# Kernel tuning notes

Measured on AMD Instinct MI355X. Metric: run time of the kernel, lower is better.

Reference implementation:

```python
import jax, jax.numpy as jnp
import numpy as np

N, K, P, D, H = 1024, 32, 1024, 512, 256
FDIM = 3 * P + 3 * D + 4  # 4612
GLOBAL_MEAN_AFFINITY = 6.5


def _init_linear(key, fan_in, fan_out):
    kw, kb = jax.random.split(key)
    bound = 1.0 / np.sqrt(fan_in)
    w = jax.random.uniform(kw, (fan_in, fan_out), jnp.float32, -bound, bound)
    b = jax.random.uniform(kb, (fan_out,), jnp.float32, -bound, bound)
    return w, b


def setup_inputs() -> dict:
    key = jax.random.key(0)
    ks = jax.random.split(key, 16)
    inp = {
        "neighbor_protein": jax.random.normal(ks[0], (N, K, P), jnp.float32),
        "neighbor_drug": jax.random.normal(ks[1], (N, K, D), jnp.float32),
        "neighbor_affinity": jax.random.normal(ks[2], (N, K), jnp.float32),
        "neighbor_ppr": jax.random.uniform(ks[3], (N, K), jnp.float32),
        "neighbor_trust": jax.random.uniform(ks[4], (N, K), jnp.float32),
        "neighbor_mask": jax.random.randint(ks[5], (N, K), 0, 2).astype(bool),
        "qry_protein": jax.random.normal(ks[6], (N, P), jnp.float32),
        "qry_drug": jax.random.normal(ks[7], (N, D), jnp.float32),
    }
    # weight_net params
    inp["w1"], inp["wb1"] = _init_linear(ks[8], FDIM, H)
    inp["w2"], inp["wb2"] = _init_linear(ks[9], H, H // 2)
    inp["w3"], inp["wb3"] = _init_linear(ks[10], H // 2, 1)
    # delta_net params
    inp["d1"], inp["db1"] = _init_linear(ks[11], FDIM, H)
    inp["d2"], inp["db2"] = _init_linear(ks[12], H, H // 2)
    inp["d3"], inp["db3"] = _init_linear(ks[13], H // 2, 1)
    # binding_encoder params (MLP over [qry_protein, qry_drug])
    inp["be1"], inp["beb1"] = _init_linear(ks[14], P + D, H)
    inp["be2"], inp["beb2"] = _init_linear(ks[15], H, 1)
    inp["log_sigma"] = jnp.zeros((1,), jnp.float32)
    return inp


def _mlp3(x, w1, b1, w2, b2, w3, b3):
    h = jax.nn.relu(x @ w1 + b1)
    h = jax.nn.relu(h @ w2 + b2)
    return (h @ w3 + b3)[..., 0]


def _cosine_sim(a, b, eps=1e-8):
    na = jnp.maximum(jnp.linalg.norm(a, axis=-1), eps)
    nb = jnp.maximum(jnp.linalg.norm(b, axis=-1), eps)
    return jnp.sum(a * b, axis=-1) / (na * nb)


def reference(neighbor_protein, neighbor_drug, neighbor_affinity, neighbor_ppr,
              neighbor_trust, neighbor_mask, qry_protein, qry_drug,
              w1, wb1, w2, wb2, w3, wb3,
              d1, db1, d2, db2, d3, db3,
              be1, beb1, be2, beb2, log_sigma):
    # --- feature build: [N, K, FDIM] ---
    qp = jnp.broadcast_to(qry_protein[:, None, :], neighbor_protein.shape)
    qd = jnp.broadcast_to(qry_drug[:, None, :], neighbor_drug.shape)
    drug_sim = _cosine_sim(qd, neighbor_drug)  # [N, K]
    features = jnp.concatenate([
        qp, neighbor_protein, qp - neighbor_protein,
        qd, neighbor_drug, qd - neighbor_drug,
        neighbor_affinity[..., None], neighbor_ppr[..., None],
        neighbor_trust[..., None], drug_sim[..., None],
    ], axis=-1)

    # --- weight net + masked softmax over K ---
    logits = _mlp3(features, w1, wb1, w2, wb2, w3, wb3)  # [N, K]
    logits = jnp.where(neighbor_mask, logits, -1e9)
    weights = jax.nn.softmax(logits, axis=1) * neighbor_mask.astype(jnp.float32)
    norm = jnp.sum(weights, axis=1, keepdims=True)
    weights = jnp.where(norm > 0, weights / jnp.maximum(norm, 1e-8),
                        jnp.zeros_like(weights))

    transfer = jnp.sum(weights * neighbor_affinity, axis=1)  # [N]
    delta = _mlp3(features, d1, db1, d2, db2, d3, db3)  # [N, K]
    correction = jnp.sum(weights * delta, axis=1)  # [N]

    # --- binding encoder prior ---
    be_in = jnp.concatenate([qry_protein, qry_drug], axis=-1)
    prior = (jax.nn.relu(be_in @ be1 + beb1) @ be2 + beb2)[..., 0] + GLOBAL_MEAN_AFFINITY

    has_neighbors = jnp.any(neighbor_mask, axis=1)  # [N]
    mu = jnp.where(has_neighbors, transfer + correction, prior)
    base_sigma = jnp.broadcast_to(jax.nn.softplus(log_sigma), mu.shape)
    sigma = base_sigma + (~has_neighbors).astype(jnp.float32) * 0.15 + 1e-4
    return mu, sigma
```

## Files before the change

### kernel.cpp

```cpp
#include <hip/hip_runtime.h>
#include <cstdint>
#include <cstddef>


typedef __attribute__((ext_vector_type(8))) short s16x8;
typedef __attribute__((ext_vector_type(4))) float f32x4;

static __device__ __forceinline__ unsigned short f2bf(float f) {
  unsigned u = __float_as_uint(f);
  u += 0x7fffu + ((u >> 16) & 1u);
  return (unsigned short)(u >> 16);
}

static __device__ __forceinline__ void glds16(const void* g, void* l) {
  __builtin_amdgcn_global_load_lds(
      (const __attribute__((address_space(1))) void*)g,
      (__attribute__((address_space(3))) void*)l, 16, 0, 0);
}

__global__ void prep_k(const float* __restrict__ qp, const float* __restrict__ qd,
                       unsigned short* __restrict__ Aq, float* __restrict__ qn,
                       const float* __restrict__ w1, const float* __restrict__ d1,
                       const float* __restrict__ be1, const float* __restrict__ w2,
                       const float* __restrict__ d2,
                       unsigned short* __restrict__ Bt1,
                       unsigned short* __restrict__ Btq,
                       unsigned short* __restrict__ Bt2c) {
  const int t = threadIdx.x;
  if (blockIdx.x < 1024) {
    const int n = blockIdx.x;
    const float4* qp4 = (const float4*)(qp + (size_t)n * 1024);
    float4 v = qp4[t];
    ushort4 o4;
    o4.x = f2bf(v.x); o4.y = f2bf(v.y); o4.z = f2bf(v.z); o4.w = f2bf(v.w);
    *(ushort4*)(Aq + (size_t)n * 1536 + t * 4) = o4;
    const float2* qd2 = (const float2*)(qd + (size_t)n * 512);
    float2 w = qd2[t];
    ushort2 o2; o2.x = f2bf(w.x); o2.y = f2bf(w.y);
    *(ushort2*)(Aq + (size_t)n * 1536 + 1024 + t * 2) = o2;
    float ss = w.x * w.x + w.y * w.y;
    #pragma unroll
    for (int m = 32; m >= 1; m >>= 1) ss += __shfl_xor(ss, m);
    __shared__ float sr[4];
    if ((t & 63) == 0) sr[t >> 6] = ss;
    __syncthreads();
    if (t == 0) qn[n] = sqrtf(sr[0] + sr[1] + sr[2] + sr[3]);
    return;
  }
  const int NB1 = 512 * 1536, NBQ = 768 * 1536, NB2 = 256 * 256;
  const int nb = gridDim.x - 1024;
  for (int idx = (blockIdx.x - 1024) * 256 + t; idx < NB1 + NBQ + NB2;
       idx += nb * 256) {
    if (idx < NB1) {
      int c = idx / 1536, j = idx - c * 1536;
      const float* W = (c < 256) ? w1 : d1;
      int cc = c & 255;
      float v;
      if (j < 1024) v = W[(1024 + j) * 256 + cc] - W[(2048 + j) * 256 + cc];
      else { int jd = j - 1024; v = W[(3584 + jd) * 256 + cc] - W[(4096 + jd) * 256 + cc]; }
      Bt1[idx] = f2bf(v);
    } else if (idx < NB1 + NBQ) {
      int i2 = idx - NB1;
      int c = i2 / 1536, j = i2 - c * 1536;
      float v;
      if (c < 512) {
        const float* W = (c < 256) ? w1 : d1;
        int cc = c & 255;
        if (j < 1024) v = W[j * 256 + cc] + W[(2048 + j) * 256 + cc];
        else { int jd = j - 1024; v = W[(3072 + jd) * 256 + cc] + W[(4096 + jd) * 256 + cc]; }
      } else {
        v = be1[j * 256 + (c - 512)];
      }
      Btq[i2] = f2bf(v);
    } else {
      int i2 = idx - NB1 - NBQ;
      int o = i2 >> 8, j = i2 & 255;
      float v = (o < 128) ? w2[j * 128 + o] : d2[j * 128 + (o - 128)];
      Bt2c[i2] = f2bf(v);
    }
  }
}

__global__ __launch_bounds__(256) void gemm0_k(
    const unsigned short* __restrict__ abf, const unsigned short* __restrict__ Bt,
    const float* __restrict__ wb1, const float* __restrict__ db1,
    const float* __restrict__ beb1, float* __restrict__ uq_out) {
  __shared__ short As[128 * 64];
  __shared__ short Bs[128 * 64];
  const int tid = threadIdx.x;
  const int l = tid & 63, w = tid >> 6;
  const int wr = w >> 1, wc = w & 1;
  const int br = blockIdx.x, bc = blockIdx.y;
  const int c0 = bc * 128;
  f32x4 acc[4][4] = {};

  for (int kt = 0; kt < 24; ++kt) {
    const int k0 = kt * 64;
    __syncthreads();
    #pragma unroll
    for (int rep = 0; rep < 4; ++rep) {
      int q = rep * 256 + tid;
      int row = q >> 3, slot = q & 7;
      int kc = slot ^ (row & 7);
      int gk = k0 + kc * 8;
      long grow = (long)br * 128 + row;
      s16x8 pk = *(const s16x8*)(abf + grow * 1536 + gk);
      *(s16x8*)(&As[q * 8]) = pk;
      s16x8 pb = *(const s16x8*)(Bt + (long)(c0 + row) * 1536 + gk);
      *(s16x8*)(&Bs[q * 8]) = pb;
    }
    __syncthreads();
    #pragma unroll
    for (int kh = 0; kh < 2; ++kh) {
      s16x8 af[4], bfr[4];
      #pragma unroll
      for (int mi = 0; mi < 4; ++mi) {
        int ra = wr * 64 + mi * 16 + (l & 15);
        int sidx = (kh * 4 + (l >> 4)) ^ (ra & 7);
        af[mi] = *(const s16x8*)(&As[ra * 64 + sidx * 8]);
      }
      #pragma unroll
      for (int ni = 0; ni < 4; ++ni) {
        int rb = wc * 64 + ni * 16 + (l & 15);
        int sidx = (kh * 4 + (l >> 4)) ^ (rb & 7);
        bfr[ni] = *(const s16x8*)(&Bs[rb * 64 + sidx * 8]);
      }
      #pragma unroll
      for (int mi = 0; mi < 4; ++mi)
        #pragma unroll
        for (int ni = 0; ni < 4; ++ni)
          acc[mi][ni] = __builtin_amdgcn_mfma_f32_16x16x32_bf16(
              af[mi], bfr[ni], acc[mi][ni], 0, 0, 0);
    }
  }
  #pragma unroll
  for (int mi = 0; mi < 4; ++mi)
    #pragma unroll
    for (int ni = 0; ni < 4; ++ni)
      #pragma unroll
      for (int r = 0; r < 4; ++r) {
        int rowl = wr * 64 + mi * 16 + (l >> 4) * 4 + r;
        int coll = wc * 64 + ni * 16 + (l & 15);
        long grow = (long)br * 128 + rowl;
        int gcol = c0 + coll;
        float b = (gcol < 256) ? wb1[gcol]
                 : (gcol < 512) ? db1[gcol - 256] : beb1[gcol - 512];
        uq_out[grow * 768 + gcol] = acc[mi][ni][r] + b;
      }
}

__global__ __launch_bounds__(512, 2) void gemm1_k(
    const float* __restrict__ Anp, const float* __restrict__ And,
    const unsigned short* __restrict__ Bt,
    const float* __restrict__ uq, const float* __restrict__ aff,
    const float* __restrict__ ppr, const float* __restrict__ trs,
    const float* __restrict__ qd, const float* __restrict__ qn,
    const float* __restrict__ w1, const float* __restrict__ d1,
    const unsigned short* __restrict__ Bt2c,
    const float* __restrict__ wb2, const float* __restrict__ db2,
    const float* __restrict__ w3, const float* __restrict__ wb3,
    const float* __restrict__ d3, const float* __restrict__ db3,
    float* __restrict__ ld) {
  __shared__ short As[2][128 * 64];
  __shared__ short Bs[2][512 * 64];
  const int tid = threadIdx.x;
  const int l = tid & 63, w = tid >> 6;
  const int wr = w >> 2, wc = w & 3;
  const long br = blockIdx.x;
  const int arow = tid >> 2, aseg = tid & 3;
  const long agrow = br * 128 + arow;
  const long an = agrow >> 5;
  const int brow = tid >> 3, bslot = tid & 7;
  const int lc = l & 15, lk = l >> 4;

  f32x4 acc[4][8] = {};
  float areg[16], qreg[16];
  float dotp = 0.f, nsp = 0.f;

  auto stageBhalf = [&](int buf, int kt, int h) {
    const int k0 = kt * 64;
    #pragma unroll
    for (int i = 0; i < 4; ++i) {
      int idx = h * 4 + i;
      int row = idx * 64 + brow;
      const unsigned short* src =
          Bt + (size_t)row * 1536 + k0 + ((bslot ^ (row & 7)) * 8);
      glds16(src, &Bs[buf][(idx * 512 + tid) * 8]);
    }
  };
  auto loadA = [&](int kt) {
    const int k0 = kt * 64 + aseg * 16;
    const float* src = (k0 < 1024) ? (Anp + agrow * 1024 + k0)
                                   : (And + agrow * 512 + (k0 - 1024));
    #pragma unroll
    for (int i = 0; i < 4; ++i) {
      float4 v = ((const float4*)src)[i];
      areg[i * 4 + 0] = v.x; areg[i * 4 + 1] = v.y;
      areg[i * 4 + 2] = v.z; areg[i * 4 + 3] = v.w;
    }
    if (kt >= 16) {
      const float* qs = qd + an * 512 + (k0 - 1024);
      #pragma unroll
      for (int i = 0; i < 4; ++i) {
        float4 v = ((const float4*)qs)[i];
        qreg[i * 4 + 0] = v.x; qreg[i * 4 + 1] = v.y;
        qreg[i * 4 + 2] = v.z; qreg[i * 4 + 3] = v.w;
      }
    }
  };
  auto writeA = [&](int buf, int kt) {
    if (kt >= 16) {
      #pragma unroll
      for (int j = 0; j < 16; ++j) {
        dotp += areg[j] * qreg[j];
        nsp  += areg[j] * areg[j];
      }
    }
    #pragma unroll
    for (int j = 0; j < 2; ++j) {
      int slot = (aseg * 2 + j) ^ (arow & 7);
      s16x8 pk;
      #pragma unroll
      for (int e = 0; e < 8; ++e) pk[e] = (short)f2bf(areg[j * 8 + e]);
      *(s16x8*)(&As[buf][arow * 64 + slot * 8]) = pk;
    }
  };

  auto rdA = [&](int cur, int kh, s16x8* af) {
    #pragma unroll
    for (int mi = 0; mi < 4; ++mi) {
      int ra = wr * 64 + mi * 16 + lc;
      int sl = (kh * 4 + lk) ^ (ra & 7);
      af[mi] = *(const s16x8*)(&As[cur][ra * 64 + sl * 8]);
    }
  };
  auto rdB = [&](int cur, int kh, int nh, s16x8* bfr) {
    #pragma unroll
    for (int ni = 0; ni < 4; ++ni) {
      int rb = wc * 128 + (nh * 4 + ni) * 16 + lc;
      int sl = (kh * 4 + lk) ^ (rb & 7);
      bfr[ni] = *(const s16x8*)(&Bs[cur][rb * 64 + sl * 8]);
    }
  };

  loadA(0);
  stageBhalf(0, 0, 0); stageBhalf(0, 0, 1);
  writeA(0, 0);
  __syncthreads();

  for (int kt = 0; kt < 24; ++kt) {
    const int cur = kt & 1, nxt = cur ^ 1;
    if (kt < 23) {
      loadA(kt + 1);
      asm volatile("s_waitcnt vmcnt(4)" ::: "memory");
    } else {
      asm volatile("s_waitcnt vmcnt(0)" ::: "memory");
    }
    asm volatile("s_waitcnt lgkmcnt(0)" ::: "memory");
    __builtin_amdgcn_s_barrier();
    __builtin_amdgcn_sched_barrier(0);

    s16x8 af[4], bfr[4];
    rdA(cur, 0, af); rdB(cur, 0, 0, bfr);
    asm volatile("s_waitcnt lgkmcnt(0)" ::: "memory");
    __builtin_amdgcn_sched_barrier(0);
    __builtin_amdgcn_s_setprio(1);
    #pragma unroll
    for (int mi = 0; mi < 4; ++mi)
      #pragma unroll
      for (int ni = 0; ni < 4; ++ni)
        acc[mi][ni] = __builtin_amdgcn_mfma_f32_16x16x32_bf16(
            af[mi], bfr[ni], acc[mi][ni], 0, 0, 0);
    __builtin_amdgcn_s_setprio(0);
    if (kt < 23) stageBhalf(nxt, kt + 1, 0);
    rdB(cur, 0, 1, bfr);
    asm volatile("s_waitcnt lgkmcnt(0)" ::: "memory");
    __builtin_amdgcn_sched_barrier(0);
    __builtin_amdgcn_s_setprio(1);
    #pragma unroll
    for (int mi = 0; mi < 4; ++mi)
      #pragma unroll
      for (int ni = 0; ni < 4; ++ni)
        acc[mi][4 + ni] = __builtin_amdgcn_mfma_f32_16x16x32_bf16(
            af[mi], bfr[ni], acc[mi][4 + ni], 0, 0, 0);
    __builtin_amdgcn_s_setprio(0);
    if (kt < 23) stageBhalf(nxt, kt + 1, 1);
    rdA(cur, 1, af); rdB(cur, 1, 0, bfr);
    asm volatile("s_waitcnt lgkmcnt(0)" ::: "memory");
    __builtin_amdgcn_sched_barrier(0);
    __builtin_amdgcn_s_setprio(1);
    #pragma unroll
    for (int mi = 0; mi < 4; ++mi)
      #pragma unroll
      for (int ni = 0; ni < 4; ++ni)
        acc[mi][ni] = __builtin_amdgcn_mfma_f32_16x16x32_bf16(
            af[mi], bfr[ni], acc[mi][ni], 0, 0, 0);
    __builtin_amdgcn_s_setprio(0);
    if (kt < 23) writeA(nxt, kt + 1);
    rdB(cur, 1, 1, bfr);
    asm volatile("s_waitcnt lgkmcnt(0)" ::: "memory");
    __builtin_amdgcn_sched_barrier(0);
    __builtin_amdgcn_s_setprio(1);
    #pragma unroll
    for (int mi = 0; mi < 4; ++mi)
      #pragma unroll
      for (int ni = 0; ni < 4; ++ni)
        acc[mi][4 + ni] = __builtin_amdgcn_mfma_f32_16x16x32_bf16(
            af[mi], bfr[ni], acc[mi][4 + ni], 0, 0, 0);
    __builtin_amdgcn_s_setprio(0);
  }

  float* simLds = (float*)&As[0][0];
  float dv = dotp, nv = nsp;
  dv += __shfl_xor(dv, 1); dv += __shfl_xor(dv, 2);
  nv += __shfl_xor(nv, 1); nv += __shfl_xor(nv, 2);
  __syncthreads();
  if (aseg == 0) {
    float qv = qn[an];
    simLds[arow] = dv / (fmaxf(qv, 1e-8f) * fmaxf(sqrtf(nv), 1e-8f));
  }
  __syncthreads();

  short* h1l = &Bs[0][0];
  #pragma unroll
  for (int mi = 0; mi < 4; ++mi) {
    #pragma unroll
    for (int r = 0; r < 4; ++r) {
      int rowl = wr * 64 + mi * 16 + lk * 4 + r;
      long grow = br * 128 + rowl;
      float sa = aff[grow], sp = ppr[grow], st = trs[grow];
      float ss = simLds[rowl];
      long n = grow >> 5;
      #pragma unroll
      for (int ni = 0; ni < 8; ++ni) {
        int gcol = wc * 128 + ni * 16 + lc;
        const float* W = (gcol < 256) ? w1 : d1;
        int cc2 = gcol & 255;
        float sv = sa * W[4608 * 256 + cc2] + sp * W[4609 * 256 + cc2]
                 + st * W[4610 * 256 + cc2] + ss * W[4611 * 256 + cc2];
        float x = acc[mi][ni][r] + uq[n * 768 + gcol] + sv;
        int chsw = (gcol >> 3) ^ (rowl & 7);
        h1l[rowl * 512 + chsw * 8 + (gcol & 7)] = (short)f2bf(fmaxf(x, 0.f));
      }
    }
  }
  __syncthreads();

  short* B2 = &As[0][0];
  f32x4 acc2[4][4] = {};
  const int rh = w >> 2;
  const int oq = w & 3;
  const int ob = oq * 64;
  const int kbase = (oq < 2) ? 0 : 256;
  for (int cc = 0; cc < 4; ++cc) {
    #pragma unroll
    for (int i = 0; i < 4; ++i) {
      int q = i * 512 + tid;
      int o = q >> 3, sl = q & 7;
      const unsigned short* src =
          Bt2c + (size_t)o * 256 + cc * 64 + ((sl ^ (o & 7)) * 8);
      glds16(src, &B2[q * 8]);
    }
    __syncthreads();
    #pragma unroll
    for (int kh = 0; kh < 2; ++kh) {
      s16x8 a2[4], b2f[4];
      #pragma unroll
      for (int mi = 0; mi < 4; ++mi) {
        int row = rh * 64 + mi * 16 + lc;
        int acol = kbase + cc * 64 + kh * 32 + lk * 8;
        int chsw = (acol >> 3) ^ (row & 7);
        a2[mi] = *(const s16x8*)(&h1l[row * 512 + chsw * 8]);
      }
      #pragma unroll
      for (int ni = 0; ni < 4; ++ni) {
        int o = ob + ni * 16 + lc;
        int sl = (kh * 4 + lk) ^ (o & 7);
        b2f[ni] = *(const s16x8*)(&B2[o * 64 + sl * 8]);
      }
      #pragma unroll
      for (int mi = 0; mi < 4; ++mi)
        #pragma unroll
        for (int ni = 0; ni < 4; ++ni)
          acc2[mi][ni] = __builtin_amdgcn_mfma_f32_16x16x32_bf16(
              a2[mi], b2f[ni], acc2[mi][ni], 0, 0, 0);
    }
    __syncthreads();
  }

  float coef[4], bb[4];
  #pragma unroll
  for (int ni = 0; ni < 4; ++ni) {
    int o = ob + ni * 16 + lc;
    coef[ni] = (o < 128) ? w3[o] : d3[o - 128];
    bb[ni]   = (o < 128) ? wb2[o] : db2[o - 128];
  }
  float* part = (float*)&As[0][0];
  #pragma unroll
  for (int mi = 0; mi < 4; ++mi) {
    #pragma unroll
    for (int rr = 0; rr < 4; ++rr) {
      float p = 0.f;
      #pragma unroll
      for (int ni = 0; ni < 4; ++ni)
        p += fmaxf(acc2[mi][ni][rr] + bb[ni], 0.f) * coef[ni];
      p += __shfl_xor(p, 1); p += __shfl_xor(p, 2);
      p += __shfl_xor(p, 4); p += __shfl_xor(p, 8);
      if (lc == 0)
        part[oq * 128 + rh * 64 + mi * 16 + lk * 4 + rr] = p;
    }
  }
  __syncthreads();
  if (tid < 256) {
    int row = tid >> 1, hf = tid & 1;
    long grow = br * 128 + row;
    float v = hf ? (part[2 * 128 + row] + part[3 * 128 + row] + db3[0])
                 : (part[0 * 128 + row] + part[1 * 128 + row] + wb3[0]);
    ld[(size_t)hf * 32768 + grow] = v;
  }
}

__global__ void finalize2_k(const float* __restrict__ uq, const float* __restrict__ ld,
                            const float* __restrict__ be2, const float* __restrict__ beb2,
                            const int* __restrict__ mask, const float* __restrict__ aff,
                            const float* __restrict__ lsg, float* __restrict__ out) {
  int n = blockIdx.x, t = threadIdx.x;
  __shared__ float s_red[4];
  float x = uq[(size_t)n * 768 + 512 + t];
  float pp = fmaxf(x, 0.f) * be2[t];
  #pragma unroll
  for (int m = 32; m >= 1; m >>= 1) pp += __shfl_xor(pp, m);
  if ((t & 63) == 0) s_red[t >> 6] = pp;
  __syncthreads();
  if (t < 64) {
    int kk = t & 31;
    int m = mask[n * 32 + kk];
    float lg = m ? ld[n * 32 + kk] : -1e9f;
    float dl = ld[32768 + n * 32 + kk];
    float mx = lg;
    #pragma unroll
    for (int mm = 16; mm >= 1; mm >>= 1) mx = fmaxf(mx, __shfl_xor(mx, mm));
    float e = expf(lg - mx);
    float s = e;
    #pragma unroll
    for (int mm = 16; mm >= 1; mm >>= 1) s += __shfl_xor(s, mm);
    float wgt = (e / s) * (m ? 1.f : 0.f);
    float nrm = wgt;
    #pragma unroll
    for (int mm = 16; mm >= 1; mm >>= 1) nrm += __shfl_xor(nrm, mm);
    wgt = (nrm > 0.f) ? wgt / fmaxf(nrm, 1e-8f) : 0.f;
    float tr = wgt * aff[n * 32 + kk];
    float co = wgt * dl;
    int am = m;
    #pragma unroll
    for (int mm = 16; mm >= 1; mm >>= 1) {
      tr += __shfl_xor(tr, mm);
      co += __shfl_xor(co, mm);
      am |= __shfl_xor(am, mm);
    }
    if (t == 0) {
      float prior = s_red[0] + s_red[1] + s_red[2] + s_red[3] + beb2[0] + 6.5f;
      float l0 = lsg[0];
      float sp = (l0 > 20.f) ? l0 : log1pf(expf(l0));
      float mu = am ? (tr + co) : prior;
      float sg = sp + (am ? 0.f : 0.15f) + 1e-4f;
      out[n] = mu;
      out[1024 + n] = sg;
    }
  }
}

extern "C" void kernel_launch(void* const* d_in, const int* in_sizes, int n_in,
                              void* d_out, int out_size, void* d_ws, size_t ws_size,
                              hipStream_t stream) {
  const float* np_ = (const float*)d_in[0];
  const float* nd_ = (const float*)d_in[1];
  const float* aff = (const float*)d_in[2];
  const float* ppr = (const float*)d_in[3];
  const float* trs = (const float*)d_in[4];
  const int*   msk = (const int*)d_in[5];
  const float* qp  = (const float*)d_in[6];
  const float* qd  = (const float*)d_in[7];
  const float* w1  = (const float*)d_in[8];
  const float* wb1 = (const float*)d_in[9];
  const float* w2  = (const float*)d_in[10];
  const float* wb2 = (const float*)d_in[11];
  const float* w3  = (const float*)d_in[12];
  const float* wb3 = (const float*)d_in[13];
  const float* d1  = (const float*)d_in[14];
  const float* db1 = (const float*)d_in[15];
  const float* d2  = (const float*)d_in[16];
  const float* db2 = (const float*)d_in[17];
  const float* d3  = (const float*)d_in[18];
  const float* db3 = (const float*)d_in[19];
  const float* be1 = (const float*)d_in[20];
  const float* beb1 = (const float*)d_in[21];
  const float* be2 = (const float*)d_in[22];
  const float* beb2 = (const float*)d_in[23];
  const float* lsg = (const float*)d_in[24];
  float* out = (float*)d_out;

  char* ws = (char*)d_ws;
  size_t off = 0;
  auto carve = [&](size_t bytes) -> void* {
    void* p = ws + off;
    off += (bytes + 511) & ~(size_t)511;
    return p;
  };
  float*          uq   = (float*)carve(1024ull * 768 * 4);
  float*          ld   = (float*)carve(2ull * 32768 * 4);
  unsigned short* Bt1  = (unsigned short*)carve(512ull * 1536 * 2);
  unsigned short* Btq  = (unsigned short*)carve(768ull * 1536 * 2);
  unsigned short* Bt2c = (unsigned short*)carve(256ull * 256 * 2);
  unsigned short* Aq   = (unsigned short*)carve(1024ull * 1536 * 2);
  float*          qn   = (float*)carve(1024ull * 4);
  (void)ws_size; (void)in_sizes; (void)n_in; (void)out_size;

  prep_k<<<3072, 256, 0, stream>>>(qp, qd, Aq, qn,
                                   w1, d1, be1, w2, d2, Bt1, Btq, Bt2c);

  gemm0_k<<<dim3(8, 6), 256, 0, stream>>>(Aq, Btq, wb1, db1, beb1, uq);

  gemm1_k<<<256, 512, 0, stream>>>(np_, nd_, Bt1, uq, aff, ppr, trs,
                                   qd, qn, w1, d1,
                                   Bt2c, wb2, db2, w3, wb3, d3, db3, ld);

  finalize2_k<<<1024, 256, 0, stream>>>(uq, ld, be2, beb2, msk, aff, lsg, out);
}
```

Measured before the change: 139.4 us.

## Use 16-wave blocks in fused gemm1 with simpler double-buffered pipeline

Doubles the fused neighbor GEMM block from 8 to 16 waves, halving each wave's tile (4x4 MFMA tiles instead of 4x8) and the per-thread A load. It also replaces the hand-scheduled split-phase pipeline, with explicit waitcnt and sched barriers, by a plain loop that prefetches the next stage and ends each iteration with __syncthreads. The second-layer GEMM and the cosine-similarity reduction are re-split for the new wave count. The aim is more latency hiding through more waves per CU, at the cost of less register-level reuse per wave and coarser synchronisation. The launch bound (1024, 4) may not be satisfiable given the large LDS footprint.

```diff
diff --git a/kernel.cpp b/kernel.cpp
--- a/kernel.cpp
+++ b/kernel.cpp
@@ -149,7 +149,7 @@
       }
 }
 
-__global__ __launch_bounds__(512, 2) void gemm1_k(
+__global__ __launch_bounds__(1024, 4) void gemm1_k(
     const float* __restrict__ Anp, const float* __restrict__ And,
     const unsigned short* __restrict__ Bt,
     const float* __restrict__ uq, const float* __restrict__ aff,
@@ -165,156 +165,97 @@
   __shared__ short Bs[2][512 * 64];
   const int tid = threadIdx.x;
   const int l = tid & 63, w = tid >> 6;
-  const int wr = w >> 2, wc = w & 3;
+  const int wr = w >> 3, wc = w & 7;
   const long br = blockIdx.x;
-  const int arow = tid >> 2, aseg = tid & 3;
+  const int arow = tid >> 3, aseg = tid & 7;
   const long agrow = br * 128 + arow;
   const long an = agrow >> 5;
-  const int brow = tid >> 3, bslot = tid & 7;
   const int lc = l & 15, lk = l >> 4;
 
-  f32x4 acc[4][8] = {};
-  float areg[16], qreg[16];
+  f32x4 acc[4][4] = {};
+  float areg[8], qreg[8];
   float dotp = 0.f, nsp = 0.f;
 
-  auto stageBhalf = [&](int buf, int kt, int h) {
+  auto stageB = [&](int buf, int kt) {
     const int k0 = kt * 64;
     #pragma unroll
     for (int i = 0; i < 4; ++i) {
-      int idx = h * 4 + i;
-      int row = idx * 64 + brow;
+      int q = i * 1024 + tid;
+      int row = q >> 3, slot = q & 7;
       const unsigned short* src =
-          Bt + (size_t)row * 1536 + k0 + ((bslot ^ (row & 7)) * 8);
-      glds16(src, &Bs[buf][(idx * 512 + tid) * 8]);
+          Bt + (size_t)row * 1536 + k0 + ((slot ^ (row & 7)) * 8);
+      glds16(src, &Bs[buf][q * 8]);
     }
   };
   auto loadA = [&](int kt) {
-    const int k0 = kt * 64 + aseg * 16;
+    const int k0 = kt * 64 + aseg * 8;
     const float* src = (k0 < 1024) ? (Anp + agrow * 1024 + k0)
                                    : (And + agrow * 512 + (k0 - 1024));
-    #pragma unroll
-    for (int i = 0; i < 4; ++i) {
-      float4 v = ((const float4*)src)[i];
-      areg[i * 4 + 0] = v.x; areg[i * 4 + 1] = v.y;
-      areg[i * 4 + 2] = v.z; areg[i * 4 + 3] = v.w;
-    }
+    float4 v0 = ((const float4*)src)[0];
+    float4 v1 = ((const float4*)src)[1];
+    areg[0] = v0.x; areg[1] = v0.y; areg[2] = v0.z; areg[3] = v0.w;
+    areg[4] = v1.x; areg[5] = v1.y; areg[6] = v1.z; areg[7] = v1.w;
     if (kt >= 16) {
       const float* qs = qd + an * 512 + (k0 - 1024);
-      #pragma unroll
-      for (int i = 0; i < 4; ++i) {
-        float4 v = ((const float4*)qs)[i];
-        qreg[i * 4 + 0] = v.x; qreg[i * 4 + 1] = v.y;
-        qreg[i * 4 + 2] = v.z; qreg[i * 4 + 3] = v.w;
-      }
+      float4 u0 = ((const float4*)qs)[0];
+      float4 u1 = ((const float4*)qs)[1];
+      qreg[0] = u0.x; qreg[1] = u0.y; qreg[2] = u0.z; qreg[3] = u0.w;
+      qreg[4] = u1.x; qreg[5] = u1.y; qreg[6] = u1.z; qreg[7] = u1.w;
     }
   };
   auto writeA = [&](int buf, int kt) {
     if (kt >= 16) {
       #pragma unroll
-      for (int j = 0; j < 16; ++j) {
+      for (int j = 0; j < 8; ++j) {
         dotp += areg[j] * qreg[j];
         nsp  += areg[j] * areg[j];
       }
     }
-    #pragma unroll
-    for (int j = 0; j < 2; ++j) {
-      int slot = (aseg * 2 + j) ^ (arow & 7);
-      s16x8 pk;
-      #pragma unroll
-      for (int e = 0; e < 8; ++e) pk[e] = (short)f2bf(areg[j * 8 + e]);
-      *(s16x8*)(&As[buf][arow * 64 + slot * 8]) = pk;
-    }
+    int slot = aseg ^ (arow & 7);
+    s16x8 pk;
+    #pragma unroll
+    for (int e = 0; e < 8; ++e) pk[e] = (short)f2bf(areg[e]);
+    *(s16x8*)(&As[buf][arow * 64 + slot * 8]) = pk;
   };
 
-  auto rdA = [&](int cur, int kh, s16x8* af) {
-    #pragma unroll
-    for (int mi = 0; mi < 4; ++mi) {
-      int ra = wr * 64 + mi * 16 + lc;
-      int sl = (kh * 4 + lk) ^ (ra & 7);
-      af[mi] = *(const s16x8*)(&As[cur][ra * 64 + sl * 8]);
-    }
-  };
-  auto rdB = [&](int cur, int kh, int nh, s16x8* bfr) {
-    #pragma unroll
-    for (int ni = 0; ni < 4; ++ni) {
-      int rb = wc * 128 + (nh * 4 + ni) * 16 + lc;
-      int sl = (kh * 4 + lk) ^ (rb & 7);
-      bfr[ni] = *(const s16x8*)(&Bs[cur][rb * 64 + sl * 8]);
-    }
-  };
-
-  loadA(0);
-  stageBhalf(0, 0, 0); stageBhalf(0, 0, 1);
-  writeA(0, 0);
+  stageB(0, 0); loadA(0); writeA(0, 0);
   __syncthreads();
 
   for (int kt = 0; kt < 24; ++kt) {
     const int cur = kt & 1, nxt = cur ^ 1;
-    if (kt < 23) {
-      loadA(kt + 1);
-      asm volatile("s_waitcnt vmcnt(4)" ::: "memory");
-    } else {
-      asm volatile("s_waitcnt vmcnt(0)" ::: "memory");
-    }
-    asm volatile("s_waitcnt lgkmcnt(0)" ::: "memory");
-    __builtin_amdgcn_s_barrier();
-    __builtin_amdgcn_sched_barrier(0);
-
-    s16x8 af[4], bfr[4];
-    rdA(cur, 0, af); rdB(cur, 0, 0, bfr);
-    asm volatile("s_waitcnt lgkmcnt(0)" ::: "memory");
-    __builtin_amdgcn_sched_barrier(0);
-    __builtin_amdgcn_s_setprio(1);
-    #pragma unroll
-    for (int mi = 0; mi < 4; ++mi)
-      #pragma unroll
-      for (int ni = 0; ni < 4; ++ni)
-        acc[mi][ni] = __builtin_amdgcn_mfma_f32_16x16x32_bf16(
-            af[mi], bfr[ni], acc[mi][ni], 0, 0, 0);
-    __builtin_amdgcn_s_setprio(0);
-    if (kt < 23) stageBhalf(nxt, kt + 1, 0);
-    rdB(cur, 0, 1, bfr);
-    asm volatile("s_waitcnt lgkmcnt(0)" ::: "memory");
-    __builtin_amdgcn_sched_barrier(0);
-    __builtin_amdgcn_s_setprio(1);
-    #pragma unroll
-    for (int mi = 0; mi < 4; ++mi)
-      #pragma unroll
-      for (int ni = 0; ni < 4; ++ni)
-        acc[mi][4 + ni] = __builtin_amdgcn_mfma_f32_16x16x32_bf16(
-            af[mi], bfr[ni], acc[mi][4 + ni], 0, 0, 0);
-    __builtin_amdgcn_s_setprio(0);
-    if (kt < 23) stageBhalf(nxt, kt + 1, 1);
-    rdA(cur, 1, af); rdB(cur, 1, 0, bfr);
-    asm volatile("s_waitcnt lgkmcnt(0)" ::: "memory");
-    __builtin_amdgcn_sched_barrier(0);
-    __builtin_amdgcn_s_setprio(1);
-    #pragma unroll
-    for (int mi = 0; mi < 4; ++mi)
-      #pragma unroll
-      for (int ni = 0; ni < 4; ++ni)
-        acc[mi][ni] = __builtin_amdgcn_mfma_f32_16x16x32_bf16(
-            af[mi], bfr[ni], acc[mi][ni], 0, 0, 0);
-    __builtin_amdgcn_s_setprio(0);
+    if (kt < 23) { stageB(nxt, kt + 1); loadA(kt + 1); }
+    #pragma unroll
+    for (int kh = 0; kh < 2; ++kh) {
+      s16x8 af[4], bfr[4];
+      #pragma unroll
+      for (int mi = 0; mi < 4; ++mi) {
+        int ra = wr * 64 + mi * 16 + lc;
+        int sl = (kh * 4 + lk) ^ (ra & 7);
+        af[mi] = *(const s16x8*)(&As[cur][ra * 64 + sl * 8]);
+      }
+      #pragma unroll
+      for (int ni = 0; ni < 4; ++ni) {
+        int rb = wc * 64 + ni * 16 + lc;
+        int sl = (kh * 4 + lk) ^ (rb & 7);
+        bfr[ni] = *(const s16x8*)(&Bs[cur][rb * 64 + sl * 8]);
+      }
+      __builtin_amdgcn_s_setprio(1);
+      #pragma unroll
+      for (int mi = 0; mi < 4; ++mi)
+        #pragma unroll
+        for (int ni = 0; ni < 4; ++ni)
+          acc[mi][ni] = __builtin_amdgcn_mfma_f32_16x16x32_bf16(
+              af[mi], bfr[ni], acc[mi][ni], 0, 0, 0);
+      __builtin_amdgcn_s_setprio(0);
+    }
     if (kt < 23) writeA(nxt, kt + 1);
-    rdB(cur, 1, 1, bfr);
-    asm volatile("s_waitcnt lgkmcnt(0)" ::: "memory");
-    __builtin_amdgcn_sched_barrier(0);
-    __builtin_amdgcn_s_setprio(1);
-    #pragma unroll
-    for (int mi = 0; mi < 4; ++mi)
-      #pragma unroll
-      for (int ni = 0; ni < 4; ++ni)
-        acc[mi][4 + ni] = __builtin_amdgcn_mfma_f32_16x16x32_bf16(
-            af[mi], bfr[ni], acc[mi][4 + ni], 0, 0, 0);
-    __builtin_amdgcn_s_setprio(0);
+    __syncthreads();
   }
 
   float* simLds = (float*)&As[0][0];
   float dv = dotp, nv = nsp;
-  dv += __shfl_xor(dv, 1); dv += __shfl_xor(dv, 2);
-  nv += __shfl_xor(nv, 1); nv += __shfl_xor(nv, 2);
-  __syncthreads();
+  dv += __shfl_xor(dv, 1); dv += __shfl_xor(dv, 2); dv += __shfl_xor(dv, 4);
+  nv += __shfl_xor(nv, 1); nv += __shfl_xor(nv, 2); nv += __shfl_xor(nv, 4);
   if (aseg == 0) {
     float qv = qn[an];
     simLds[arow] = dv / (fmaxf(qv, 1e-8f) * fmaxf(sqrtf(nv), 1e-8f));
@@ -332,8 +273,8 @@
       float ss = simLds[rowl];
       long n = grow >> 5;
       #pragma unroll
-      for (int ni = 0; ni < 8; ++ni) {
-        int gcol = wc * 128 + ni * 16 + lc;
+      for (int ni = 0; ni < 4; ++ni) {
+        int gcol = wc * 64 + ni * 16 + lc;
         const float* W = (gcol < 256) ? w1 : d1;
         int cc2 = gcol & 255;
         float sv = sa * W[4608 * 256 + cc2] + sp * W[4609 * 256 + cc2]
@@ -347,15 +288,15 @@
   __syncthreads();
 
   short* B2 = &As[0][0];
-  f32x4 acc2[4][4] = {};
-  const int rh = w >> 2;
+  f32x4 acc2[2][4] = {};
+  const int rq = w >> 2;
   const int oq = w & 3;
   const int ob = oq * 64;
   const int kbase = (oq < 2) ? 0 : 256;
   for (int cc = 0; cc < 4; ++cc) {
     #pragma unroll
-    for (int i = 0; i < 4; ++i) {
-      int q = i * 512 + tid;
+    for (int i = 0; i < 2; ++i) {
+      int q = i * 1024 + tid;
       int o = q >> 3, sl = q & 7;
       const unsigned short* src =
           Bt2c + (size_t)o * 256 + cc * 64 + ((sl ^ (o & 7)) * 8);
@@ -364,10 +305,10 @@
     __syncthreads();
     #pragma unroll
     for (int kh = 0; kh < 2; ++kh) {
-      s16x8 a2[4], b2f[4];
-      #pragma unroll
-      for (int mi = 0; mi < 4; ++mi) {
-        int row = rh * 64 + mi * 16 + lc;
+      s16x8 a2[2], b2f[4];
+      #pragma unroll
+      for (int mi = 0; mi < 2; ++mi) {
+        int row = rq * 32 + mi * 16 + lc;
         int acol = kbase + cc * 64 + kh * 32 + lk * 8;
         int chsw = (acol >> 3) ^ (row & 7);
         a2[mi] = *(const s16x8*)(&h1l[row * 512 + chsw * 8]);
@@ -379,7 +320,7 @@
         b2f[ni] = *(const s16x8*)(&B2[o * 64 + sl * 8]);
       }
       #pragma unroll
-      for (int mi = 0; mi < 4; ++mi)
+      for (int mi = 0; mi < 2; ++mi)
         #pragma unroll
         for (int ni = 0; ni < 4; ++ni)
           acc2[mi][ni] = __builtin_amdgcn_mfma_f32_16x16x32_bf16(
@@ -397,7 +338,7 @@
   }
   float* part = (float*)&As[0][0];
   #pragma unroll
-  for (int mi = 0; mi < 4; ++mi) {
+  for (int mi = 0; mi < 2; ++mi) {
     #pragma unroll
     for (int rr = 0; rr < 4; ++rr) {
       float p = 0.f;
@@ -407,7 +348,7 @@
       p += __shfl_xor(p, 1); p += __shfl_xor(p, 2);
       p += __shfl_xor(p, 4); p += __shfl_xor(p, 8);
       if (lc == 0)
-        part[oq * 128 + rh * 64 + mi * 16 + lk * 4 + rr] = p;
+        part[oq * 128 + rq * 32 + mi * 16 + lk * 4 + rr] = p;
     }
   }
   __syncthreads();
@@ -521,9 +462,9 @@
 
   gemm0_k<<<dim3(8, 6), 256, 0, stream>>>(Aq, Btq, wb1, db1, beb1, uq);
 
-  gemm1_k<<<256, 512, 0, stream>>>(np_, nd_, Bt1, uq, aff, ppr, trs,
-                                   qd, qn, w1, d1,
-                                   Bt2c, wb2, db2, w3, wb3, d3, db3, ld);
+  gemm1_k<<<256, 1024, 0, stream>>>(np_, nd_, Bt1, uq, aff, ppr, trs,
+                                    qd, qn, w1, d1,
+                                    Bt2c, wb2, db2, w3, wb3, d3, db3, ld);
 
   finalize2_k<<<1024, 256, 0, stream>>>(uq, ld, be2, beb2, msk, aff, lsg, out);
 }
```

After: 181.5 us. 1.3x slower.

## Fuse finalize into gemm1 epilogue and retile gemm0 to smaller tiles

Applied to the files above, without the earlier changes.

The masked softmax, transfer/correction reduction and binding-encoder prior move into the tail of gemm1, so the separate finalize kernel launch and the ld workspace round trip go away. Each gemm1 block covers 128 rows, which is 4 queries, and two waves handle them. gemm0 moves from 128x128 to 64x64 tiles (192 blocks instead of 48) and loads into LDS with global_load_lds, to fill more CUs. The trade-off is less register reuse per block in gemm0 and a longer serial tail in gemm1.

```diff
diff --git a/kernel.cpp b/kernel.cpp
--- a/kernel.cpp
+++ b/kernel.cpp
@@ -85,68 +85,52 @@
     const unsigned short* __restrict__ abf, const unsigned short* __restrict__ Bt,
     const float* __restrict__ wb1, const float* __restrict__ db1,
     const float* __restrict__ beb1, float* __restrict__ uq_out) {
-  __shared__ short As[128 * 64];
-  __shared__ short Bs[128 * 64];
+  __shared__ short As[64 * 64];
+  __shared__ short Bs[64 * 64];
   const int tid = threadIdx.x;
   const int l = tid & 63, w = tid >> 6;
-  const int wr = w >> 1, wc = w & 1;
   const int br = blockIdx.x, bc = blockIdx.y;
-  const int c0 = bc * 128;
-  f32x4 acc[4][4] = {};
+  const int c0 = bc * 64;
+  const int lc = l & 15, lk = l >> 4;
+  f32x4 acc[4] = {};
 
   for (int kt = 0; kt < 24; ++kt) {
     const int k0 = kt * 64;
     __syncthreads();
     #pragma unroll
-    for (int rep = 0; rep < 4; ++rep) {
-      int q = rep * 256 + tid;
+    for (int i = 0; i < 2; ++i) {
+      int q = i * 256 + tid;
       int row = q >> 3, slot = q & 7;
-      int kc = slot ^ (row & 7);
-      int gk = k0 + kc * 8;
-      long grow = (long)br * 128 + row;
-      s16x8 pk = *(const s16x8*)(abf + grow * 1536 + gk);
-      *(s16x8*)(&As[q * 8]) = pk;
-      s16x8 pb = *(const s16x8*)(Bt + (long)(c0 + row) * 1536 + gk);
-      *(s16x8*)(&Bs[q * 8]) = pb;
+      int sw = (slot ^ (row & 7)) * 8;
+      glds16(abf + (size_t)(br * 64 + row) * 1536 + k0 + sw, &As[q * 8]);
+      glds16(Bt + (size_t)(c0 + row) * 1536 + k0 + sw, &Bs[q * 8]);
     }
     __syncthreads();
     #pragma unroll
     for (int kh = 0; kh < 2; ++kh) {
-      s16x8 af[4], bfr[4];
-      #pragma unroll
-      for (int mi = 0; mi < 4; ++mi) {
-        int ra = wr * 64 + mi * 16 + (l & 15);
-        int sidx = (kh * 4 + (l >> 4)) ^ (ra & 7);
-        af[mi] = *(const s16x8*)(&As[ra * 64 + sidx * 8]);
-      }
+      int ra = w * 16 + lc;
+      int sla = (kh * 4 + lk) ^ (ra & 7);
+      s16x8 af = *(const s16x8*)(&As[ra * 64 + sla * 8]);
       #pragma unroll
       for (int ni = 0; ni < 4; ++ni) {
-        int rb = wc * 64 + ni * 16 + (l & 15);
-        int sidx = (kh * 4 + (l >> 4)) ^ (rb & 7);
-        bfr[ni] = *(const s16x8*)(&Bs[rb * 64 + sidx * 8]);
-      }
-      #pragma unroll
-      for (int mi = 0; mi < 4; ++mi)
-        #pragma unroll
-        for (int ni = 0; ni < 4; ++ni)
-          acc[mi][ni] = __builtin_amdgcn_mfma_f32_16x16x32_bf16(
-              af[mi], bfr[ni], acc[mi][ni], 0, 0, 0);
+        int rb = ni * 16 + lc;
+        int slb = (kh * 4 + lk) ^ (rb & 7);
+        s16x8 bf = *(const s16x8*)(&Bs[rb * 64 + slb * 8]);
+        acc[ni] = __builtin_amdgcn_mfma_f32_16x16x32_bf16(af, bf, acc[ni], 0, 0, 0);
+      }
     }
   }
   #pragma unroll
-  for (int mi = 0; mi < 4; ++mi)
-    #pragma unroll
-    for (int ni = 0; ni < 4; ++ni)
-      #pragma unroll
-      for (int r = 0; r < 4; ++r) {
-        int rowl = wr * 64 + mi * 16 + (l >> 4) * 4 + r;
-        int coll = wc * 64 + ni * 16 + (l & 15);
-        long grow = (long)br * 128 + rowl;
-        int gcol = c0 + coll;
-        float b = (gcol < 256) ? wb1[gcol]
-                 : (gcol < 512) ? db1[gcol - 256] : beb1[gcol - 512];
-        uq_out[grow * 768 + gcol] = acc[mi][ni][r] + b;
-      }
+  for (int ni = 0; ni < 4; ++ni)
+    #pragma unroll
+    for (int r = 0; r < 4; ++r) {
+      int rowl = w * 16 + lk * 4 + r;
+      int gcol = c0 + ni * 16 + lc;
+      long grow = (long)br * 64 + rowl;
+      float b = (gcol < 256) ? wb1[gcol]
+               : (gcol < 512) ? db1[gcol - 256] : beb1[gcol - 512];
+      uq_out[grow * 768 + gcol] = acc[ni][r] + b;
+    }
 }
 
 __global__ __launch_bounds__(512, 2) void gemm1_k(
@@ -160,7 +144,9 @@
     const float* __restrict__ wb2, const float* __restrict__ db2,
     const float* __restrict__ w3, const float* __restrict__ wb3,
     const float* __restrict__ d3, const float* __restrict__ db3,
-    float* __restrict__ ld) {
+    const int* __restrict__ msk, const float* __restrict__ be2,
+    const float* __restrict__ beb2, const float* __restrict__ lsg,
+    float* __restrict__ out) {
   __shared__ short As[2][128 * 64];
   __shared__ short Bs[2][512 * 64];
   const int tid = threadIdx.x;
@@ -411,32 +397,22 @@
     }
   }
   __syncthreads();
-  if (tid < 256) {
-    int row = tid >> 1, hf = tid & 1;
-    long grow = br * 128 + row;
-    float v = hf ? (part[2 * 128 + row] + part[3 * 128 + row] + db3[0])
-                 : (part[0 * 128 + row] + part[1 * 128 + row] + wb3[0]);
-    ld[(size_t)hf * 32768 + grow] = v;
-  }
-}
-
-__global__ void finalize2_k(const float* __restrict__ uq, const float* __restrict__ ld,
-                            const float* __restrict__ be2, const float* __restrict__ beb2,
-                            const int* __restrict__ mask, const float* __restrict__ aff,
-                            const float* __restrict__ lsg, float* __restrict__ out) {
-  int n = blockIdx.x, t = threadIdx.x;
-  __shared__ float s_red[4];
-  float x = uq[(size_t)n * 768 + 512 + t];
-  float pp = fmaxf(x, 0.f) * be2[t];
-  #pragma unroll
-  for (int m = 32; m >= 1; m >>= 1) pp += __shfl_xor(pp, m);
-  if ((t & 63) == 0) s_red[t >> 6] = pp;
-  __syncthreads();
-  if (t < 64) {
-    int kk = t & 31;
-    int m = mask[n * 32 + kk];
-    float lg = m ? ld[n * 32 + kk] : -1e9f;
-    float dl = ld[32768 + n * 32 + kk];
+
+  if (w < 2) {
+    const int half = l >> 5, kk = l & 31;
+    const int rowl = (w * 2 + half) * 32 + kk;
+    const long n = br * 4 + w * 2 + half;
+    float lgt = part[0 * 128 + rowl] + part[1 * 128 + rowl] + wb3[0];
+    float dlt = part[2 * 128 + rowl] + part[3 * 128 + rowl] + db3[0];
+    float pp = 0.f;
+    const float* uqr = uq + (size_t)n * 768 + 512 + kk * 8;
+    #pragma unroll
+    for (int j = 0; j < 8; ++j)
+      pp += fmaxf(uqr[j], 0.f) * be2[kk * 8 + j];
+    #pragma unroll
+    for (int mm = 16; mm >= 1; mm >>= 1) pp += __shfl_xor(pp, mm);
+    int m = msk[n * 32 + kk];
+    float lg = m ? lgt : -1e9f;
     float mx = lg;
     #pragma unroll
     for (int mm = 16; mm >= 1; mm >>= 1) mx = fmaxf(mx, __shfl_xor(mx, mm));
@@ -450,7 +426,7 @@
     for (int mm = 16; mm >= 1; mm >>= 1) nrm += __shfl_xor(nrm, mm);
     wgt = (nrm > 0.f) ? wgt / fmaxf(nrm, 1e-8f) : 0.f;
     float tr = wgt * aff[n * 32 + kk];
-    float co = wgt * dl;
+    float co = wgt * dlt;
     int am = m;
     #pragma unroll
     for (int mm = 16; mm >= 1; mm >>= 1) {
@@ -458,14 +434,12 @@
       co += __shfl_xor(co, mm);
       am |= __shfl_xor(am, mm);
     }
-    if (t == 0) {
-      float prior = s_red[0] + s_red[1] + s_red[2] + s_red[3] + beb2[0] + 6.5f;
+    if (kk == 0) {
+      float prior = pp + beb2[0] + 6.5f;
       float l0 = lsg[0];
       float sp = (l0 > 20.f) ? l0 : log1pf(expf(l0));
-      float mu = am ? (tr + co) : prior;
-      float sg = sp + (am ? 0.f : 0.15f) + 1e-4f;
-      out[n] = mu;
-      out[1024 + n] = sg;
+      out[n] = am ? (tr + co) : prior;
+      out[1024 + n] = sp + (am ? 0.f : 0.15f) + 1e-4f;
     }
   }
 }
@@ -508,7 +482,6 @@
     return p;
   };
   float*          uq   = (float*)carve(1024ull * 768 * 4);
-  float*          ld   = (float*)carve(2ull * 32768 * 4);
   unsigned short* Bt1  = (unsigned short*)carve(512ull * 1536 * 2);
   unsigned short* Btq  = (unsigned short*)carve(768ull * 1536 * 2);
   unsigned short* Bt2c = (unsigned short*)carve(256ull * 256 * 2);
@@ -519,11 +492,10 @@
   prep_k<<<3072, 256, 0, stream>>>(qp, qd, Aq, qn,
                                    w1, d1, be1, w2, d2, Bt1, Btq, Bt2c);
 
-  gemm0_k<<<dim3(8, 6), 256, 0, stream>>>(Aq, Btq, wb1, db1, beb1, uq);
+  gemm0_k<<<dim3(16, 12), 256, 0, stream>>>(Aq, Btq, wb1, db1, beb1, uq);
 
   gemm1_k<<<256, 512, 0, stream>>>(np_, nd_, Bt1, uq, aff, ppr, trs,
                                    qd, qn, w1, d1,
-                                   Bt2c, wb2, db2, w3, wb3, d3, db3, ld);
-
-  finalize2_k<<<1024, 256, 0, stream>>>(uq, ld, be2, beb2, msk, aff, lsg, out);
+                                   Bt2c, wb2, db2, w3, wb3, d3, db3,
+                                   msk, be2, beb2, lsg, out);
 }
```

Measured after the change: 124.3 us (median of 2 runs). 1.12x faster.
